# Optimization experiments

Hardware: AMD Instinct MI355X
Metric: run time of the kernel (lower is better)

Reference implementation:

```python
import jax, jax.numpy as jnp
import numpy as np

# FP4 E2M1 lookup: low 3 bits -> magnitude {0,.5,1,1.5,2,3,4,6}, bit 3 -> sign
FP4_LUT = jnp.array([0.0, 0.5, 1.0, 1.5, 2.0, 3.0, 4.0, 6.0,
                     -0.0, -0.5, -1.0, -1.5, -2.0, -3.0, -4.0, -6.0], dtype=jnp.float32)


def _dequant(packed_i32, scales, group_size):
    """packed_i32: [K/8, N] (8 FP4 nibbles per word along K); scales: [K/group_size, N] fp16.
    Returns dense [K, N] float32 weight."""
    p = packed_i32.astype(jnp.uint32)
    shifts = (jnp.arange(8, dtype=jnp.uint32) * jnp.uint32(4))
    nib = ((p[:, None, :] >> shifts[None, :, None]) & jnp.uint32(0xF)).astype(jnp.int32)  # [K/8,8,N]
    K = p.shape[0] * 8
    vals = FP4_LUT[nib.reshape(K, p.shape[1])]  # [K, N] f32
    g = jnp.arange(K) // group_size
    return vals * scales.astype(jnp.float32)[g]


def setup_inputs() -> dict:
    key = jax.random.key(0)
    k1, k2, k3, k4, k5 = jax.random.split(key, 5)
    B, H, I, G = 32, 4096, 2048, 128
    x = (jax.random.normal(k1, (B, H), dtype=jnp.float32) * 0.5).astype(jnp.float16)
    gate_up_packed = jax.random.bits(k2, (H // 8, 2 * I), dtype=jnp.uint32).astype(jnp.int32)
    down_packed = jax.random.bits(k3, (I // 8, H), dtype=jnp.uint32).astype(jnp.int32)
    gate_up_scales = (jax.random.uniform(k4, (H // G, 2 * I), minval=0.005, maxval=0.02)).astype(jnp.float16)
    down_scales = (jax.random.uniform(k5, (I // G, H), minval=0.005, maxval=0.02)).astype(jnp.float16)
    return {"x": x, "gate_up_packed": gate_up_packed, "gate_up_scales": gate_up_scales,
            "down_packed": down_packed, "down_scales": down_scales, "group_size": G}


def reference(x, gate_up_packed, gate_up_scales, down_packed, down_scales, group_size):
    w_gu = _dequant(gate_up_packed, gate_up_scales, group_size)   # [H, 2I]
    h = jnp.einsum('bh,hn->bn', x.astype(jnp.float32), w_gu)      # [B, 2I]
    inter = h.shape[1] // 2
    act = jax.nn.silu(h[:, :inter]) * h[:, inter:]                # SwiGLU
    w_d = _dequant(down_packed, down_scales, group_size)          # [I, H]
    out = jnp.einsum('bi,ih->bh', act, w_d)
    return out.astype(jnp.float16)
```

## Files before the change

kernel.cpp:

```cpp
#include <hip/hip_runtime.h>
#include <cstdint>

typedef float f32x4 __attribute__((ext_vector_type(4)));

constexpr int Bv = 32;
constexpr int Hv = 4096;
constexpr int Iv = 2048;
constexpr int N1 = 4096;

__device__ __forceinline__ long dec8(uint32_t w) {
  uint32_t lo = w & 0x07070707u;
  uint32_t hi = (w >> 4) & 0x07070707u;
  uint32_t me = __builtin_amdgcn_perm(0x4C484440u, 0x3C383000u, lo);
  uint32_t mo = __builtin_amdgcn_perm(0x4C484440u, 0x3C383000u, hi);
  uint32_t e  = me | ((w & 0x08080808u) << 4);
  uint32_t o  = mo | (w & 0x80808080u);
  uint32_t d0 = __builtin_amdgcn_perm(o, e, 0x05010400u);
  uint32_t d1 = __builtin_amdgcn_perm(o, e, 0x07030602u);
  return (long)(((uint64_t)d1 << 32) | d0);
}

__device__ __forceinline__ void quant8(const float* p, long& hi, long& lo) {
  f32x4 a = *(const f32x4*)p;
  f32x4 b = *(const f32x4*)(p + 4);
  uint32_t h0 = 0, h1 = 0;
  h0 = __builtin_amdgcn_cvt_pk_fp8_f32(a[0], a[1], h0, false);
  h0 = __builtin_amdgcn_cvt_pk_fp8_f32(a[2], a[3], h0, true);
  h1 = __builtin_amdgcn_cvt_pk_fp8_f32(b[0], b[1], h1, false);
  h1 = __builtin_amdgcn_cvt_pk_fp8_f32(b[2], b[3], h1, true);
  float r0 = a[0] - __builtin_amdgcn_cvt_f32_fp8(h0, 0);
  float r1 = a[1] - __builtin_amdgcn_cvt_f32_fp8(h0, 1);
  float r2 = a[2] - __builtin_amdgcn_cvt_f32_fp8(h0, 2);
  float r3 = a[3] - __builtin_amdgcn_cvt_f32_fp8(h0, 3);
  float r4 = b[0] - __builtin_amdgcn_cvt_f32_fp8(h1, 0);
  float r5 = b[1] - __builtin_amdgcn_cvt_f32_fp8(h1, 1);
  float r6 = b[2] - __builtin_amdgcn_cvt_f32_fp8(h1, 2);
  float r7 = b[3] - __builtin_amdgcn_cvt_f32_fp8(h1, 3);
  uint32_t l0 = 0, l1 = 0;
  l0 = __builtin_amdgcn_cvt_pk_fp8_f32(r0, r1, l0, false);
  l0 = __builtin_amdgcn_cvt_pk_fp8_f32(r2, r3, l0, true);
  l1 = __builtin_amdgcn_cvt_pk_fp8_f32(r4, r5, l1, false);
  l1 = __builtin_amdgcn_cvt_pk_fp8_f32(r6, r7, l1, true);
  hi = (long)(((uint64_t)h1 << 32) | h0);
  lo = (long)(((uint64_t)l1 << 32) | l0);
}

__global__ __launch_bounds__(1024, 4) void k_gateup(
    const float* __restrict__ x, const uint32_t* __restrict__ wp,
    const float* __restrict__ sc, float* __restrict__ hp) {
  __shared__ float lds[16 * 1024];
  const int nt = blockIdx.x >> 1;
  const int kh = blockIdx.x & 1;
  const int wid = threadIdx.x >> 6, lane = threadIdx.x & 63;
  const int q = lane >> 4, r = lane & 15;
  const int n0 = nt * 32;
  const int nA = n0 + r, nB = n0 + 16 + r;

  const int koff = kh * 2048 + wid * 128 + q * 8;
  const float* px0 = x + r * Hv + koff;
  const float* px1 = x + (r + 16) * Hv + koff;
  const uint32_t* pbA = wp + (size_t)(kh * 256 + wid * 16 + q) * N1 + nA;
  const uint32_t* pbB = pbA + 16;

  f32x4 t00 = {0,0,0,0}, t01 = {0,0,0,0}, t10 = {0,0,0,0}, t11 = {0,0,0,0};
  #pragma unroll
  for (int st = 0; st < 4; ++st) {
    long A0h, A0l, A1h, A1l;
    quant8(px0 + st * 32, A0h, A0l);
    quant8(px1 + st * 32, A1h, A1l);
    long BA = dec8(pbA[(size_t)st * 4 * N1]);
    long BB = dec8(pbB[(size_t)st * 4 * N1]);
    t00 = __builtin_amdgcn_mfma_f32_16x16x32_fp8_fp8(A0h, BA, t00, 0, 0, 0);
    t00 = __builtin_amdgcn_mfma_f32_16x16x32_fp8_fp8(A0l, BA, t00, 0, 0, 0);
    t01 = __builtin_amdgcn_mfma_f32_16x16x32_fp8_fp8(A0h, BB, t01, 0, 0, 0);
    t01 = __builtin_amdgcn_mfma_f32_16x16x32_fp8_fp8(A0l, BB, t01, 0, 0, 0);
    t10 = __builtin_amdgcn_mfma_f32_16x16x32_fp8_fp8(A1h, BA, t10, 0, 0, 0);
    t10 = __builtin_amdgcn_mfma_f32_16x16x32_fp8_fp8(A1l, BA, t10, 0, 0, 0);
    t11 = __builtin_amdgcn_mfma_f32_16x16x32_fp8_fp8(A1h, BB, t11, 0, 0, 0);
    t11 = __builtin_amdgcn_mfma_f32_16x16x32_fp8_fp8(A1l, BB, t11, 0, 0, 0);
  }
  const int g = kh * 16 + wid;
  const float sA = sc[g * N1 + nA];
  const float sB = sc[g * N1 + nB];
  float* my = lds + wid * 1024;
  #pragma unroll
  for (int j = 0; j < 4; ++j) {
    const int rw = q * 4 + j;
    my[rw * 32 + r]             = sA * t00[j];
    my[rw * 32 + 16 + r]        = sB * t01[j];
    my[(16 + rw) * 32 + r]      = sA * t10[j];
    my[(16 + rw) * 32 + 16 + r] = sB * t11[j];
  }
  __syncthreads();
  const int i = threadIdx.x;
  float sum = 0.f;
  #pragma unroll
  for (int w = 0; w < 16; ++w) sum += lds[w * 1024 + i];
  hp[(size_t)kh * (Bv * N1) + (i >> 5) * N1 + n0 + (i & 31)] = sum;
}

__global__ __launch_bounds__(64) void k_swiglu(const float* __restrict__ hp,
                                               uint32_t* __restrict__ ah,
                                               uint32_t* __restrict__ al) {
  const int t = blockIdx.x * 64 + threadIdx.x;
  const int m = t >> 9;
  const int c = (t & 511) * 4;
  constexpr int P = Bv * N1;
  const float* pg = hp + m * N1 + c;
  const float* pu = pg + Iv;
  f32x4 g = *(const f32x4*)pg + *(const f32x4*)(pg + P);
  f32x4 u = *(const f32x4*)pu + *(const f32x4*)(pu + P);
  float a[4];
  #pragma unroll
  for (int j = 0; j < 4; ++j) {
    float gv = g[j];
    float av = gv / (1.0f + __expf(-gv)) * u[j];
    a[j] = fminf(fmaxf(av, -440.0f), 440.0f);
  }
  uint32_t h = 0;
  h = __builtin_amdgcn_cvt_pk_fp8_f32(a[0], a[1], h, false);
  h = __builtin_amdgcn_cvt_pk_fp8_f32(a[2], a[3], h, true);
  float r0 = a[0] - __builtin_amdgcn_cvt_f32_fp8(h, 0);
  float r1 = a[1] - __builtin_amdgcn_cvt_f32_fp8(h, 1);
  float r2 = a[2] - __builtin_amdgcn_cvt_f32_fp8(h, 2);
  float r3 = a[3] - __builtin_amdgcn_cvt_f32_fp8(h, 3);
  uint32_t l = 0;
  l = __builtin_amdgcn_cvt_pk_fp8_f32(r0, r1, l, false);
  l = __builtin_amdgcn_cvt_pk_fp8_f32(r2, r3, l, true);
  ah[t] = h; al[t] = l;
}

__global__ __launch_bounds__(1024, 4) void k_down(
    const uint8_t* __restrict__ ah8, const uint8_t* __restrict__ al8,
    const uint32_t* __restrict__ wp, const float* __restrict__ sc,
    float* __restrict__ out) {
  __shared__ float lds[16 * 512];
  const int n0 = blockIdx.x * 16;
  const int wid = threadIdx.x >> 6, lane = threadIdx.x & 63;
  const int q = lane >> 4, r = lane & 15;
  const int n = n0 + r;

  const int koff = wid * 128 + q * 8;
  const uint8_t* pa0h = ah8 + r * Iv + koff;
  const uint8_t* pa0l = al8 + r * Iv + koff;
  const uint8_t* pa1h = ah8 + (r + 16) * Iv + koff;
  const uint8_t* pa1l = al8 + (r + 16) * Iv + koff;
  const uint32_t* pb = wp + (size_t)(wid * 16 + q) * Hv + n;

  f32x4 t0 = {0,0,0,0}, t1 = {0,0,0,0};
  #pragma unroll
  for (int st = 0; st < 4; ++st) {
    long A0h = *(const long*)(pa0h + st * 32);
    long A0l = *(const long*)(pa0l + st * 32);
    long A1h = *(const long*)(pa1h + st * 32);
    long A1l = *(const long*)(pa1l + st * 32);
    long Bf = dec8(pb[(size_t)st * 4 * Hv]);
    t0 = __builtin_amdgcn_mfma_f32_16x16x32_fp8_fp8(A0h, Bf, t0, 0, 0, 0);
    t0 = __builtin_amdgcn_mfma_f32_16x16x32_fp8_fp8(A0l, Bf, t0, 0, 0, 0);
    t1 = __builtin_amdgcn_mfma_f32_16x16x32_fp8_fp8(A1h, Bf, t1, 0, 0, 0);
    t1 = __builtin_amdgcn_mfma_f32_16x16x32_fp8_fp8(A1l, Bf, t1, 0, 0, 0);
  }
  const float sv = sc[wid * Hv + n];
  float* my = lds + wid * 512;
  #pragma unroll
  for (int j = 0; j < 4; ++j) {
    const int rw = q * 4 + j;
    my[rw * 16 + r]        = sv * t0[j];
    my[(16 + rw) * 16 + r] = sv * t1[j];
  }
  __syncthreads();
  const int i = threadIdx.x;
  if (i < 512) {
    float sum = 0.f;
    #pragma unroll
    for (int w = 0; w < 16; ++w) sum += lds[w * 512 + i];
    out[(i >> 4) * N1 + n0 + (i & 15)] = sum;
  }
}

extern "C" void kernel_launch(void* const* d_in, const int* in_sizes, int n_in,
                              void* d_out, int out_size, void* d_ws, size_t ws_size,
                              hipStream_t stream) {
  const float*    x   = (const float*)d_in[0];
  const uint32_t* gup = (const uint32_t*)d_in[1];
  const float*    gus = (const float*)d_in[2];
  const uint32_t* dnp = (const uint32_t*)d_in[3];
  const float*    dns = (const float*)d_in[4];

  float*   hp  = (float*)d_ws;
  uint8_t* a8h = (uint8_t*)d_ws + 2*(size_t)Bv*N1*sizeof(float);
  uint8_t* a8l = a8h + Bv*Iv;

  k_gateup<<<256, 1024, 0, stream>>>(x, gup, gus, hp);
  k_swiglu<<<256,   64, 0, stream>>>(hp, (uint32_t*)a8h, (uint32_t*)a8l);
  k_down  <<<256, 1024, 0, stream>>>(a8h, a8l, dnp, dns, (float*)d_out);
}
```

Baseline: 91.27 us.

## Switch MFMA path from split FP8 hi/lo to single FP16 operands

Replaces the two-pass FP8 emulation (hi and residual lo FP8 operands, two MFMAs per tile) with a single FP16 MFMA per tile. FP4 weights are now decoded directly to FP16 via byte permutes, and activations are packed with round-toward-zero FP16 conversion. The SwiGLU kernel writes one FP16 activation buffer instead of two FP8 buffers and runs half as many blocks, each doing eight elements. This halves the MFMA count and simplifies conversion work, but FP16 MFMA has a lower issue rate than FP8 and the activation traffic is the same size. The old clamp before quantisation is removed, so values outside FP16 range could overflow.

New measurement: 88.09 us. 1.04x faster.

```diff
diff --git a/kernel.cpp b/kernel.cpp
--- a/kernel.cpp
+++ b/kernel.cpp
@@ -2,47 +2,40 @@
 #include <cstdint>
 
 typedef float f32x4 __attribute__((ext_vector_type(4)));
+typedef float f32x2 __attribute__((ext_vector_type(2)));
+typedef __fp16 f16;
+typedef f16 f16x2 __attribute__((ext_vector_type(2)));
+typedef f16 f16x8 __attribute__((ext_vector_type(8)));
 
 constexpr int Bv = 32;
 constexpr int Hv = 4096;
 constexpr int Iv = 2048;
 constexpr int N1 = 4096;
 
-__device__ __forceinline__ long dec8(uint32_t w) {
+__device__ __forceinline__ f16x8 dec8h(uint32_t w) {
   uint32_t lo = w & 0x07070707u;
   uint32_t hi = (w >> 4) & 0x07070707u;
-  uint32_t me = __builtin_amdgcn_perm(0x4C484440u, 0x3C383000u, lo);
-  uint32_t mo = __builtin_amdgcn_perm(0x4C484440u, 0x3C383000u, hi);
-  uint32_t e  = me | ((w & 0x08080808u) << 4);
-  uint32_t o  = mo | (w & 0x80808080u);
-  uint32_t d0 = __builtin_amdgcn_perm(o, e, 0x05010400u);
-  uint32_t d1 = __builtin_amdgcn_perm(o, e, 0x07030602u);
-  return (long)(((uint64_t)d1 << 32) | d0);
+  uint32_t e = __builtin_amdgcn_perm(0x46444240u, 0x3E3C3800u, lo)
+             | ((w & 0x08080808u) << 4);
+  uint32_t o = __builtin_amdgcn_perm(0x46444240u, 0x3E3C3800u, hi)
+             | (w & 0x80808080u);
+  union { uint32_t u[4]; f16x8 v; } r;
+  r.u[0] = __builtin_amdgcn_perm(e, 0u, 0x05000400u);
+  r.u[1] = __builtin_amdgcn_perm(e, 0u, 0x07000600u);
+  r.u[2] = __builtin_amdgcn_perm(o, 0u, 0x05000400u);
+  r.u[3] = __builtin_amdgcn_perm(o, 0u, 0x07000600u);
+  return r.v;
 }
 
-__device__ __forceinline__ void quant8(const float* p, long& hi, long& lo) {
+__device__ __forceinline__ f16x8 packA(const float* p) {
   f32x4 a = *(const f32x4*)p;
   f32x4 b = *(const f32x4*)(p + 4);
-  uint32_t h0 = 0, h1 = 0;
-  h0 = __builtin_amdgcn_cvt_pk_fp8_f32(a[0], a[1], h0, false);
-  h0 = __builtin_amdgcn_cvt_pk_fp8_f32(a[2], a[3], h0, true);
-  h1 = __builtin_amdgcn_cvt_pk_fp8_f32(b[0], b[1], h1, false);
-  h1 = __builtin_amdgcn_cvt_pk_fp8_f32(b[2], b[3], h1, true);
-  float r0 = a[0] - __builtin_amdgcn_cvt_f32_fp8(h0, 0);
-  float r1 = a[1] - __builtin_amdgcn_cvt_f32_fp8(h0, 1);
-  float r2 = a[2] - __builtin_amdgcn_cvt_f32_fp8(h0, 2);
-  float r3 = a[3] - __builtin_amdgcn_cvt_f32_fp8(h0, 3);
-  float r4 = b[0] - __builtin_amdgcn_cvt_f32_fp8(h1, 0);
-  float r5 = b[1] - __builtin_amdgcn_cvt_f32_fp8(h1, 1);
-  float r6 = b[2] - __builtin_amdgcn_cvt_f32_fp8(h1, 2);
-  float r7 = b[3] - __builtin_amdgcn_cvt_f32_fp8(h1, 3);
-  uint32_t l0 = 0, l1 = 0;
-  l0 = __builtin_amdgcn_cvt_pk_fp8_f32(r0, r1, l0, false);
-  l0 = __builtin_amdgcn_cvt_pk_fp8_f32(r2, r3, l0, true);
-  l1 = __builtin_amdgcn_cvt_pk_fp8_f32(r4, r5, l1, false);
-  l1 = __builtin_amdgcn_cvt_pk_fp8_f32(r6, r7, l1, true);
-  hi = (long)(((uint64_t)h1 << 32) | h0);
-  lo = (long)(((uint64_t)l1 << 32) | l0);
+  union { f16x2 h[4]; f16x8 v; } r;
+  r.h[0] = __builtin_amdgcn_cvt_pkrtz(a[0], a[2]);
+  r.h[1] = __builtin_amdgcn_cvt_pkrtz(b[0], b[2]);
+  r.h[2] = __builtin_amdgcn_cvt_pkrtz(a[1], a[3]);
+  r.h[3] = __builtin_amdgcn_cvt_pkrtz(b[1], b[3]);
+  return r.v;
 }
 
 __global__ __launch_bounds__(1024, 4) void k_gateup(
@@ -65,19 +58,14 @@
   f32x4 t00 = {0,0,0,0}, t01 = {0,0,0,0}, t10 = {0,0,0,0}, t11 = {0,0,0,0};
   #pragma unroll
   for (int st = 0; st < 4; ++st) {
-    long A0h, A0l, A1h, A1l;
-    quant8(px0 + st * 32, A0h, A0l);
-    quant8(px1 + st * 32, A1h, A1l);
-    long BA = dec8(pbA[(size_t)st * 4 * N1]);
-    long BB = dec8(pbB[(size_t)st * 4 * N1]);
-    t00 = __builtin_amdgcn_mfma_f32_16x16x32_fp8_fp8(A0h, BA, t00, 0, 0, 0);
-    t00 = __builtin_amdgcn_mfma_f32_16x16x32_fp8_fp8(A0l, BA, t00, 0, 0, 0);
-    t01 = __builtin_amdgcn_mfma_f32_16x16x32_fp8_fp8(A0h, BB, t01, 0, 0, 0);
-    t01 = __builtin_amdgcn_mfma_f32_16x16x32_fp8_fp8(A0l, BB, t01, 0, 0, 0);
-    t10 = __builtin_amdgcn_mfma_f32_16x16x32_fp8_fp8(A1h, BA, t10, 0, 0, 0);
-    t10 = __builtin_amdgcn_mfma_f32_16x16x32_fp8_fp8(A1l, BA, t10, 0, 0, 0);
-    t11 = __builtin_amdgcn_mfma_f32_16x16x32_fp8_fp8(A1h, BB, t11, 0, 0, 0);
-    t11 = __builtin_amdgcn_mfma_f32_16x16x32_fp8_fp8(A1l, BB, t11, 0, 0, 0);
+    f16x8 A0 = packA(px0 + st * 32);
+    f16x8 A1 = packA(px1 + st * 32);
+    f16x8 BA = dec8h(pbA[(size_t)st * 4 * N1]);
+    f16x8 BB = dec8h(pbB[(size_t)st * 4 * N1]);
+    t00 = __builtin_amdgcn_mfma_f32_16x16x32_f16(A0, BA, t00, 0, 0, 0);
+    t01 = __builtin_amdgcn_mfma_f32_16x16x32_f16(A0, BB, t01, 0, 0, 0);
+    t10 = __builtin_amdgcn_mfma_f32_16x16x32_f16(A1, BA, t10, 0, 0, 0);
+    t11 = __builtin_amdgcn_mfma_f32_16x16x32_f16(A1, BB, t11, 0, 0, 0);
   }
   const int g = kh * 16 + wid;
   const float sA = sc[g * N1 + nA];
@@ -100,40 +88,39 @@
 }
 
 __global__ __launch_bounds__(64) void k_swiglu(const float* __restrict__ hp,
-                                               uint32_t* __restrict__ ah,
-                                               uint32_t* __restrict__ al) {
+                                               uint4* __restrict__ act) {
   const int t = blockIdx.x * 64 + threadIdx.x;
-  const int m = t >> 9;
-  const int c = (t & 511) * 4;
+  const int m = t >> 8;
+  const int c = (t & 255) * 8;
   constexpr int P = Bv * N1;
   const float* pg = hp + m * N1 + c;
   const float* pu = pg + Iv;
-  f32x4 g = *(const f32x4*)pg + *(const f32x4*)(pg + P);
-  f32x4 u = *(const f32x4*)pu + *(const f32x4*)(pu + P);
-  float a[4];
+  f32x4 g0 = *(const f32x4*)pg       + *(const f32x4*)(pg + P);
+  f32x4 g1 = *(const f32x4*)(pg + 4) + *(const f32x4*)(pg + 4 + P);
+  f32x4 u0 = *(const f32x4*)pu       + *(const f32x4*)(pu + P);
+  f32x4 u1 = *(const f32x4*)(pu + 4) + *(const f32x4*)(pu + 4 + P);
+  float a[8];
   #pragma unroll
   for (int j = 0; j < 4; ++j) {
-    float gv = g[j];
-    float av = gv / (1.0f + __expf(-gv)) * u[j];
-    a[j] = fminf(fmaxf(av, -440.0f), 440.0f);
+    float gv = g0[j];
+    a[j] = gv / (1.0f + __expf(-gv)) * u0[j];
   }
-  uint32_t h = 0;
-  h = __builtin_amdgcn_cvt_pk_fp8_f32(a[0], a[1], h, false);
-  h = __builtin_amdgcn_cvt_pk_fp8_f32(a[2], a[3], h, true);
-  float r0 = a[0] - __builtin_amdgcn_cvt_f32_fp8(h, 0);
-  float r1 = a[1] - __builtin_amdgcn_cvt_f32_fp8(h, 1);
-  float r2 = a[2] - __builtin_amdgcn_cvt_f32_fp8(h, 2);
-  float r3 = a[3] - __builtin_amdgcn_cvt_f32_fp8(h, 3);
-  uint32_t l = 0;
-  l = __builtin_amdgcn_cvt_pk_fp8_f32(r0, r1, l, false);
-  l = __builtin_amdgcn_cvt_pk_fp8_f32(r2, r3, l, true);
-  ah[t] = h; al[t] = l;
+  #pragma unroll
+  for (int j = 0; j < 4; ++j) {
+    float gv = g1[j];
+    a[4 + j] = gv / (1.0f + __expf(-gv)) * u1[j];
+  }
+  union { f16x2 h[4]; uint4 u; } r;
+  r.h[0] = __builtin_amdgcn_cvt_pkrtz(a[0], a[2]);
+  r.h[1] = __builtin_amdgcn_cvt_pkrtz(a[4], a[6]);
+  r.h[2] = __builtin_amdgcn_cvt_pkrtz(a[1], a[3]);
+  r.h[3] = __builtin_amdgcn_cvt_pkrtz(a[5], a[7]);
+  act[t] = r.u;
 }
 
 __global__ __launch_bounds__(1024, 4) void k_down(
-    const uint8_t* __restrict__ ah8, const uint8_t* __restrict__ al8,
-    const uint32_t* __restrict__ wp, const float* __restrict__ sc,
-    float* __restrict__ out) {
+    const f16* __restrict__ act, const uint32_t* __restrict__ wp,
+    const float* __restrict__ sc, float* __restrict__ out) {
   __shared__ float lds[16 * 512];
   const int n0 = blockIdx.x * 16;
   const int wid = threadIdx.x >> 6, lane = threadIdx.x & 63;
@@ -141,24 +128,18 @@
   const int n = n0 + r;
 
   const int koff = wid * 128 + q * 8;
-  const uint8_t* pa0h = ah8 + r * Iv + koff;
-  const uint8_t* pa0l = al8 + r * Iv + koff;
-  const uint8_t* pa1h = ah8 + (r + 16) * Iv + koff;
-  const uint8_t* pa1l = al8 + (r + 16) * Iv + koff;
+  const f16* pa0 = act + r * Iv + koff;
+  const f16* pa1 = act + (r + 16) * Iv + koff;
   const uint32_t* pb = wp + (size_t)(wid * 16 + q) * Hv + n;
 
   f32x4 t0 = {0,0,0,0}, t1 = {0,0,0,0};
   #pragma unroll
   for (int st = 0; st < 4; ++st) {
-    long A0h = *(const long*)(pa0h + st * 32);
-    long A0l = *(const long*)(pa0l + st * 32);
-    long A1h = *(const long*)(pa1h + st * 32);
-    long A1l = *(const long*)(pa1l + st * 32);
-    long Bf = dec8(pb[(size_t)st * 4 * Hv]);
-    t0 = __builtin_amdgcn_mfma_f32_16x16x32_fp8_fp8(A0h, Bf, t0, 0, 0, 0);
-    t0 = __builtin_amdgcn_mfma_f32_16x16x32_fp8_fp8(A0l, Bf, t0, 0, 0, 0);
-    t1 = __builtin_amdgcn_mfma_f32_16x16x32_fp8_fp8(A1h, Bf, t1, 0, 0, 0);
-    t1 = __builtin_amdgcn_mfma_f32_16x16x32_fp8_fp8(A1l, Bf, t1, 0, 0, 0);
+    f16x8 A0 = *(const f16x8*)(pa0 + st * 32);
+    f16x8 A1 = *(const f16x8*)(pa1 + st * 32);
+    f16x8 B  = dec8h(pb[(size_t)st * 4 * Hv]);
+    t0 = __builtin_amdgcn_mfma_f32_16x16x32_f16(A0, B, t0, 0, 0, 0);
+    t1 = __builtin_amdgcn_mfma_f32_16x16x32_f16(A1, B, t1, 0, 0, 0);
   }
   const float sv = sc[wid * Hv + n];
   float* my = lds + wid * 512;
@@ -187,11 +168,10 @@
   const uint32_t* dnp = (const uint32_t*)d_in[3];
   const float*    dns = (const float*)d_in[4];
 
-  float*   hp  = (float*)d_ws;
-  uint8_t* a8h = (uint8_t*)d_ws + 2*(size_t)Bv*N1*sizeof(float);
-  uint8_t* a8l = a8h + Bv*Iv;
+  float* hp  = (float*)d_ws;
+  f16*   act = (f16*)((char*)d_ws + 2 * (size_t)Bv * N1 * sizeof(float));
 
   k_gateup<<<256, 1024, 0, stream>>>(x, gup, gus, hp);
-  k_swiglu<<<256,   64, 0, stream>>>(hp, (uint32_t*)a8h, (uint32_t*)a8l);
-  k_down  <<<256, 1024, 0, stream>>>(a8h, a8l, dnp, dns, (float*)d_out);
+  k_swiglu<<<128,   64, 0, stream>>>(hp, (uint4*)act);
+  k_down  <<<256, 1024, 0, stream>>>(act, dnp, dns, (float*)d_out);
 }
```
